# Kernel optimization log

Hardware: AMD Instinct MI355X
Metric: run time of the kernel (lower is better)

## Reference

```python
import jax, jax.numpy as jnp
import numpy as np
import math

NUM_WORDS = 8192
WORD_WIDTH = 512
PROJ_WIDTH = 64
NUM_HEADS = 8
SCALE_FACTOR = 100.0

def setup_inputs() -> dict:
    key = jax.random.key(0)
    kx, kq, kk, kv, ko = jax.random.split(key, 5)
    x = jax.random.normal(kx, (NUM_WORDS, WORD_WIDTH), dtype=jnp.float32)
    w_q = jax.random.normal(kq, (WORD_WIDTH, PROJ_WIDTH), dtype=jnp.float32) / SCALE_FACTOR
    w_k = jax.random.normal(kk, (WORD_WIDTH, PROJ_WIDTH), dtype=jnp.float32) / SCALE_FACTOR
    w_v = jax.random.normal(kv, (WORD_WIDTH, PROJ_WIDTH), dtype=jnp.float32) / SCALE_FACTOR
    w_o = jax.random.normal(ko, (WORD_WIDTH, WORD_WIDTH), dtype=jnp.float32)
    return {"x": x, "w_q": w_q, "w_k": w_k, "w_v": w_v, "w_o": w_o}

def reference(x, w_q, w_k, w_v, w_o):
    # Single self-attention head (all 8 heads in the source share the same weights).
    q = x @ w_q            # [N, P]
    k = x @ w_k            # [N, P]
    v = x @ w_v            # [N, P]
    scores = jax.nn.softmax((q @ k.T) / jnp.sqrt(jnp.float32(q.shape[1])), axis=1)  # [N, N]
    head = scores @ v      # [N, P]
    # concat of NUM_HEADS identical head outputs along dim=1
    concat = jnp.tile(head, (1, NUM_HEADS))  # [N, NUM_HEADS*P]
    return concat @ w_o    # [N, WORD_WIDTH]
```

## Files before the change

kernel.cpp:

```cpp
#include <hip/hip_runtime.h>
#include <stdint.h>

#define N_WORDS 8192
#define LOG2E_8 0.18033688011112043f

typedef __attribute__((ext_vector_type(8))) short short8;
typedef __attribute__((ext_vector_type(4))) float f32x4;
typedef __attribute__((ext_vector_type(4))) _Float16 half4;

__device__ __forceinline__ unsigned short f32_to_bf16(float f) {
    union { float f; unsigned u; } v; v.f = f;
    unsigned u = v.u;
    return (unsigned short)((u + 0x7FFFu + ((u >> 16) & 1u)) >> 16);
}

__device__ __forceinline__ unsigned short f32_to_f16(float f) {
    union { _Float16 h; unsigned short u; } cv;
    cv.h = (_Float16)f;
    return cv.u;
}

__device__ __forceinline__ void async16(const void* g, void* l) {
    __builtin_amdgcn_global_load_lds(
        (const __attribute__((address_space(1))) unsigned int*)g,
        (__attribute__((address_space(3))) unsigned int*)l, 16, 0, 0);
}

__global__ __launch_bounds__(256) void qkv_gemm(
    const float* __restrict__ x,
    const float* __restrict__ wq, const float* __restrict__ wk,
    const float* __restrict__ wv,
    unsigned short* __restrict__ qB, unsigned short* __restrict__ kB,
    unsigned short* __restrict__ vH)
{
    __shared__ __align__(16) unsigned short ldsX[64 * 72];
    __shared__ __align__(16) unsigned short ldsW[64 * 72];

    int t = threadIdx.x;
    int mt = blockIdx.x;
    int mat = blockIdx.y;
    const float* w = (mat == 0) ? wq : (mat == 1) ? wk : wv;

    int wvid = t >> 6, lane = t & 63;
    int lq = lane & 15, quad = lane >> 4;

    f32x4 acc[4];
#pragma unroll
    for (int nt = 0; nt < 4; ++nt) acc[nt] = (f32x4){0.f, 0.f, 0.f, 0.f};

    for (int kb = 0; kb < 8; ++kb) {
        int k0 = kb * 64;
        __syncthreads();
#pragma unroll
        for (int j = 0; j < 4; ++j) {
            int i = t + j * 256;
            int row = i >> 4, c4 = (i & 15) * 4;
            float4 xv = *(const float4*)(x + (size_t)(mt * 64 + row) * 512 + k0 + c4);
            unsigned p0 = f32_to_bf16(xv.x) | ((unsigned)f32_to_bf16(xv.y) << 16);
            unsigned p1 = f32_to_bf16(xv.z) | ((unsigned)f32_to_bf16(xv.w) << 16);
            *(uint2*)(&ldsX[row * 72 + c4]) = make_uint2(p0, p1);
        }
        {
            int n = t & 63, kbs = (t >> 6) * 16;
#pragma unroll
            for (int kk = 0; kk < 16; kk += 2) {
                float a = w[(size_t)(k0 + kbs + kk) * 64 + n];
                float b = w[(size_t)(k0 + kbs + kk + 1) * 64 + n];
                unsigned p = f32_to_bf16(a) | ((unsigned)f32_to_bf16(b) << 16);
                *(unsigned*)(&ldsW[n * 72 + kbs + kk]) = p;
            }
        }
        __syncthreads();

        int m = wvid * 16 + lq;
        short8 a0 = *(const short8*)(&ldsX[m * 72 + quad * 8]);
        short8 a1 = *(const short8*)(&ldsX[m * 72 + 32 + quad * 8]);
#pragma unroll
        for (int nt = 0; nt < 4; ++nt) {
            short8 b0 = *(const short8*)(&ldsW[(nt * 16 + lq) * 72 + quad * 8]);
            short8 b1 = *(const short8*)(&ldsW[(nt * 16 + lq) * 72 + 32 + quad * 8]);
            acc[nt] = __builtin_amdgcn_mfma_f32_16x16x32_bf16(a0, b0, acc[nt], 0, 0, 0);
            acc[nt] = __builtin_amdgcn_mfma_f32_16x16x32_bf16(a1, b1, acc[nt], 0, 0, 0);
        }
    }

    int mrow_base = mt * 64 + wvid * 16;
#pragma unroll
    for (int nt = 0; nt < 4; ++nt) {
#pragma unroll
        for (int r = 0; r < 4; ++r) {
            int row = mrow_base + quad * 4 + r;
            int n = nt * 16 + lq;
            float v = acc[nt][r];
            if (mat == 0) {
                v *= LOG2E_8;
                int col = ((((n >> 3) ^ (row & 7)) << 3)) | (n & 7);
                qB[(size_t)row * 64 + col] = f32_to_bf16(v);
            } else if (mat == 1) {
                int col = ((((n >> 3) ^ (row & 7)) << 3)) | (n & 7);
                kB[(size_t)row * 64 + col] = f32_to_bf16(v);
            } else {
                int rs = (row & ~63) | (((((row >> 3) & 7) ^ (n & 7)) << 3)) | (row & 7);
                vH[(size_t)n * N_WORDS + rs] = f32_to_f16(v);
            }
        }
    }
}

__global__ __launch_bounds__(256) void woeff_kernel(
    const float* __restrict__ wo, float* __restrict__ we)
{
    int i = blockIdx.x * 256 + threadIdx.x;
    int p = i >> 9;
    int j = i & 511;
    float s = 0.0f;
#pragma unroll
    for (int h = 0; h < 8; ++h) s += wo[(size_t)(h * 64 + p) * 512 + j];
    we[i] = s;
}

__global__ __launch_bounds__(256) void attn_kernel(
    const unsigned short* __restrict__ qB,
    const unsigned short* __restrict__ kB,
    const unsigned short* __restrict__ vH,
    float* __restrict__ pO, float* __restrict__ pl, int nk)
{
    __shared__ __align__(16) unsigned short ldsK[128 * 64];
    __shared__ __align__(16) unsigned short ldsV[64 * 128];

    int t = threadIdx.x;
    int wvid = t >> 6, lane = t & 63;
    int lq = lane & 15, quad = lane >> 4;
    int mbase = blockIdx.x * 128 + wvid * 32;
    int n0 = blockIdx.y * nk;

    short8 qf[2][2];
#pragma unroll
    for (int qs = 0; qs < 2; ++qs) {
        int row = mbase + qs * 16 + lq;
        const unsigned short* qr = qB + (size_t)row * 64;
        int s7 = row & 7;
        qf[qs][0] = *(const short8*)(qr + ((quad ^ s7) << 3));
        qf[qs][1] = *(const short8*)(qr + (((4 + quad) ^ s7) << 3));
    }

    f32x4 oacc[2][4];
#pragma unroll
    for (int qs = 0; qs < 2; ++qs)
#pragma unroll
        for (int vt = 0; vt < 4; ++vt) oacc[qs][vt] = (f32x4){0.f, 0.f, 0.f, 0.f};
    float lsum0 = 0.f, lsum1 = 0.f;

    int tiles = nk >> 7;
    for (int tt = 0; tt < tiles; ++tt) {
        int nb = n0 + tt * 128;
        __syncthreads();
        {
            const char* gK = (const char*)kB + (size_t)nb * 128;
#pragma unroll
            for (int i = 0; i < 4; ++i) {
                int L0 = (wvid * 4 + i) * 64;
                async16(gK + (size_t)(L0 + lane) * 16, (char*)ldsK + (size_t)L0 * 16);
            }
#pragma unroll
            for (int i = 0; i < 4; ++i) {
                int L0 = (wvid * 4 + i) * 64;
                int L = L0 + lane;
                int vcol = L >> 4, ct = L & 15;
                const char* src = (const char*)vH + (size_t)vcol * 16384 +
                                  (size_t)nb * 2 + ((ct >> 3) << 7) + ((ct & 7) << 4);
                async16(src, (char*)ldsV + (size_t)L0 * 16);
            }
        }
        __syncthreads();

#pragma unroll 2
        for (int nt = 0; nt < 8; ++nt) {
            int s7 = lq & 7;
            const unsigned short* kr = ldsK + (nt * 16 + lq) * 64;
            short8 a0 = *(const short8*)(kr + ((quad ^ s7) << 3));
            short8 a1 = *(const short8*)(kr + (((4 + quad) ^ s7) << 3));
            f32x4 st0 = (f32x4){0.f, 0.f, 0.f, 0.f};
            f32x4 st1 = (f32x4){0.f, 0.f, 0.f, 0.f};
            st0 = __builtin_amdgcn_mfma_f32_16x16x32_bf16(a0, qf[0][0], st0, 0, 0, 0);
            st0 = __builtin_amdgcn_mfma_f32_16x16x32_bf16(a1, qf[0][1], st0, 0, 0, 0);
            st1 = __builtin_amdgcn_mfma_f32_16x16x32_bf16(a0, qf[1][0], st1, 0, 0, 0);
            st1 = __builtin_amdgcn_mfma_f32_16x16x32_bf16(a1, qf[1][1], st1, 0, 0, 0);

            half4 p0, p1;
#pragma unroll
            for (int r = 0; r < 4; ++r) {
                float e = exp2f(st0[r]);
                lsum0 += e;
                p0[r] = (_Float16)e;
            }
#pragma unroll
            for (int r = 0; r < 4; ++r) {
                float e = exp2f(st1[r]);
                lsum1 += e;
                p1[r] = (_Float16)e;
            }

            int ct = nt * 2 + (quad >> 1);
            int off = (quad & 1) * 4;
#pragma unroll
            for (int vt = 0; vt < 4; ++vt) {
                int vcol = vt * 16 + lq;
                int cs = (ct & 8) | ((ct & 7) ^ (vcol & 7));
                half4 vb = *(const half4*)(ldsV + vcol * 128 + (cs << 3) + off);
                oacc[0][vt] = __builtin_amdgcn_mfma_f32_16x16x16f16(p0, vb, oacc[0][vt], 0, 0, 0);
                oacc[1][vt] = __builtin_amdgcn_mfma_f32_16x16x16f16(p1, vb, oacc[1][vt], 0, 0, 0);
            }
        }
    }

    lsum0 += __shfl_xor(lsum0, 16); lsum0 += __shfl_xor(lsum0, 32);
    lsum1 += __shfl_xor(lsum1, 16); lsum1 += __shfl_xor(lsum1, 32);

    size_t obase = (size_t)blockIdx.y * N_WORDS;
    if (quad == 0) {
        pl[obase + mbase + lq] = lsum0;
        pl[obase + mbase + 16 + lq] = lsum1;
    }
#pragma unroll
    for (int qs = 0; qs < 2; ++qs)
#pragma unroll
        for (int vt = 0; vt < 4; ++vt)
#pragma unroll
            for (int r = 0; r < 4; ++r) {
                int row = mbase + qs * 16 + quad * 4 + r;
                pO[(obase + row) * 64 + vt * 16 + lq] = oacc[qs][vt][r];
            }
}

__global__ __launch_bounds__(256) void combine_kernel(
    const float* __restrict__ pO, const float* __restrict__ pl,
    float* __restrict__ head, int S)
{
    int i = blockIdx.x * 256 + threadIdx.x;
    int row = i >> 6, d = i & 63;
    float so = 0.f, sl = 0.f;
    for (int s = 0; s < S; ++s) {
        so += pO[((size_t)s * N_WORDS + row) * 64 + d];
        sl += pl[(size_t)s * N_WORDS + row];
    }
    head[i] = so / sl;
}

__global__ __launch_bounds__(256) void out_kernel(
    const float* __restrict__ head, const float* __restrict__ we,
    float* __restrict__ out)
{
    __shared__ __align__(16) float ldsHT[64 * 16];
    int t = threadIdx.x;
    int r0 = blockIdx.x * 16;
    {
        int r = t >> 4, c4 = (t & 15) * 4;
        float4 hv = *(const float4*)(head + (size_t)(r0 + r) * 64 + c4);
        ldsHT[(c4 + 0) * 16 + r] = hv.x;
        ldsHT[(c4 + 1) * 16 + r] = hv.y;
        ldsHT[(c4 + 2) * 16 + r] = hv.z;
        ldsHT[(c4 + 3) * 16 + r] = hv.w;
    }
    __syncthreads();

    int w = t >> 6, l = t & 63;
    int cg = w & 1, rg = w >> 1;
    int j0 = cg * 256 + l * 4;

    float4 acc[8];
#pragma unroll
    for (int rr = 0; rr < 8; ++rr) acc[rr] = (float4){0.f, 0.f, 0.f, 0.f};

    for (int k = 0; k < 64; ++k) {
        float4 wv = *(const float4*)(we + (size_t)k * 512 + j0);
        float4 h0 = *(const float4*)(ldsHT + k * 16 + rg * 8);
        float4 h1 = *(const float4*)(ldsHT + k * 16 + rg * 8 + 4);
        float hr[8] = {h0.x, h0.y, h0.z, h0.w, h1.x, h1.y, h1.z, h1.w};
#pragma unroll
        for (int rr = 0; rr < 8; ++rr) {
            acc[rr].x = fmaf(hr[rr], wv.x, acc[rr].x);
            acc[rr].y = fmaf(hr[rr], wv.y, acc[rr].y);
            acc[rr].z = fmaf(hr[rr], wv.z, acc[rr].z);
            acc[rr].w = fmaf(hr[rr], wv.w, acc[rr].w);
        }
    }

#pragma unroll
    for (int rr = 0; rr < 8; ++rr) {
        int row = r0 + rg * 8 + rr;
        *(float4*)(out + (size_t)row * 512 + j0) = acc[rr];
    }
}

extern "C" void kernel_launch(void* const* d_in, const int* in_sizes, int n_in,
                              void* d_out, int out_size, void* d_ws, size_t ws_size,
                              hipStream_t stream)
{
    const float* x  = (const float*)d_in[0];
    const float* wq = (const float*)d_in[1];
    const float* wk = (const float*)d_in[2];
    const float* wv = (const float*)d_in[3];
    const float* wo = (const float*)d_in[4];
    float* out = (float*)d_out;

    char* ws = (char*)d_ws;
    unsigned short* qB = (unsigned short*)(ws);
    unsigned short* kB = (unsigned short*)(ws + 1048576);
    unsigned short* vH = (unsigned short*)(ws + 2097152);
    float* we   = (float*)(ws + 3145728);
    float* head = (float*)(ws + 3276800);
    float* pl   = (float*)(ws + 5373952);
    float* pO   = (float*)(ws + 5636096);

    int S = (ws_size >= (size_t)(5636096) + 8u * 2097152u) ? 8 : 4;
    int nk = N_WORDS / S;

    hipLaunchKernelGGL(qkv_gemm, dim3(128, 3), dim3(256), 0, stream,
                       x, wq, wk, wv, qB, kB, vH);
    hipLaunchKernelGGL(woeff_kernel, dim3(128), dim3(256), 0, stream, wo, we);
    hipLaunchKernelGGL(attn_kernel, dim3(64, S), dim3(256), 0, stream,
                       qB, kB, vH, pO, pl, nk);
    hipLaunchKernelGGL(combine_kernel, dim3(2048), dim3(256), 0, stream,
                       pO, pl, head, S);
    hipLaunchKernelGGL(out_kernel, dim3(512), dim3(256), 0, stream,
                       head, we, out);
}
```

Measured before the change: 136.9 us.

## Pre-convert inputs, double-buffer QKV and attention loads, fuse combine into output GEMM

Adds separate kernels that convert x and the Q/K/V weights to swizzled bf16 once. The QKV GEMM now computes all three projections per 16-row block and stages tiles through double-buffered async LDS copies. The attention kernel moves to 64-key tiles with double-buffered K/V staging, so the next tile's loads overlap the current tile's compute. The combine kernel is folded into the output projection, dropping one launch and the head round trip, at the cost of two extra prep launches and more workspace.

```diff
diff --git a/kernel.cpp b/kernel.cpp
--- a/kernel.cpp
+++ b/kernel.cpp
@@ -26,85 +26,41 @@
         (__attribute__((address_space(3))) unsigned int*)l, 16, 0, 0);
 }
 
-__global__ __launch_bounds__(256) void qkv_gemm(
-    const float* __restrict__ x,
+__global__ __launch_bounds__(256) void xcvt_kernel(
+    const float* __restrict__ x, unsigned short* __restrict__ xb)
+{
+    int ci = blockIdx.x * 256 + threadIdx.x;
+    int row = ci >> 6, c = ci & 63;
+    const float* src = x + ((size_t)row * 512 + c * 8);
+    float4 v0 = *(const float4*)(src);
+    float4 v1 = *(const float4*)(src + 4);
+    unsigned u0 = f32_to_bf16(v0.x) | ((unsigned)f32_to_bf16(v0.y) << 16);
+    unsigned u1 = f32_to_bf16(v0.z) | ((unsigned)f32_to_bf16(v0.w) << 16);
+    unsigned u2 = f32_to_bf16(v1.x) | ((unsigned)f32_to_bf16(v1.y) << 16);
+    unsigned u3 = f32_to_bf16(v1.z) | ((unsigned)f32_to_bf16(v1.w) << 16);
+    int dst = (c & ~7) | ((c ^ (row & 7)) & 7);
+    *(uint4*)(xb + (size_t)row * 512 + dst * 8) = make_uint4(u0, u1, u2, u3);
+}
+
+__global__ __launch_bounds__(192) void wprep_kernel(
     const float* __restrict__ wq, const float* __restrict__ wk,
-    const float* __restrict__ wv,
-    unsigned short* __restrict__ qB, unsigned short* __restrict__ kB,
-    unsigned short* __restrict__ vH)
-{
-    __shared__ __align__(16) unsigned short ldsX[64 * 72];
-    __shared__ __align__(16) unsigned short ldsW[64 * 72];
-
-    int t = threadIdx.x;
-    int mt = blockIdx.x;
-    int mat = blockIdx.y;
-    const float* w = (mat == 0) ? wq : (mat == 1) ? wk : wv;
-
-    int wvid = t >> 6, lane = t & 63;
-    int lq = lane & 15, quad = lane >> 4;
-
-    f32x4 acc[4];
-#pragma unroll
-    for (int nt = 0; nt < 4; ++nt) acc[nt] = (f32x4){0.f, 0.f, 0.f, 0.f};
-
-    for (int kb = 0; kb < 8; ++kb) {
-        int k0 = kb * 64;
-        __syncthreads();
-#pragma unroll
-        for (int j = 0; j < 4; ++j) {
-            int i = t + j * 256;
-            int row = i >> 4, c4 = (i & 15) * 4;
-            float4 xv = *(const float4*)(x + (size_t)(mt * 64 + row) * 512 + k0 + c4);
-            unsigned p0 = f32_to_bf16(xv.x) | ((unsigned)f32_to_bf16(xv.y) << 16);
-            unsigned p1 = f32_to_bf16(xv.z) | ((unsigned)f32_to_bf16(xv.w) << 16);
-            *(uint2*)(&ldsX[row * 72 + c4]) = make_uint2(p0, p1);
-        }
-        {
-            int n = t & 63, kbs = (t >> 6) * 16;
-#pragma unroll
-            for (int kk = 0; kk < 16; kk += 2) {
-                float a = w[(size_t)(k0 + kbs + kk) * 64 + n];
-                float b = w[(size_t)(k0 + kbs + kk + 1) * 64 + n];
-                unsigned p = f32_to_bf16(a) | ((unsigned)f32_to_bf16(b) << 16);
-                *(unsigned*)(&ldsW[n * 72 + kbs + kk]) = p;
-            }
-        }
-        __syncthreads();
-
-        int m = wvid * 16 + lq;
-        short8 a0 = *(const short8*)(&ldsX[m * 72 + quad * 8]);
-        short8 a1 = *(const short8*)(&ldsX[m * 72 + 32 + quad * 8]);
-#pragma unroll
-        for (int nt = 0; nt < 4; ++nt) {
-            short8 b0 = *(const short8*)(&ldsW[(nt * 16 + lq) * 72 + quad * 8]);
-            short8 b1 = *(const short8*)(&ldsW[(nt * 16 + lq) * 72 + 32 + quad * 8]);
-            acc[nt] = __builtin_amdgcn_mfma_f32_16x16x32_bf16(a0, b0, acc[nt], 0, 0, 0);
-            acc[nt] = __builtin_amdgcn_mfma_f32_16x16x32_bf16(a1, b1, acc[nt], 0, 0, 0);
-        }
-    }
-
-    int mrow_base = mt * 64 + wvid * 16;
-#pragma unroll
-    for (int nt = 0; nt < 4; ++nt) {
-#pragma unroll
-        for (int r = 0; r < 4; ++r) {
-            int row = mrow_base + quad * 4 + r;
-            int n = nt * 16 + lq;
-            float v = acc[nt][r];
-            if (mat == 0) {
-                v *= LOG2E_8;
-                int col = ((((n >> 3) ^ (row & 7)) << 3)) | (n & 7);
-                qB[(size_t)row * 64 + col] = f32_to_bf16(v);
-            } else if (mat == 1) {
-                int col = ((((n >> 3) ^ (row & 7)) << 3)) | (n & 7);
-                kB[(size_t)row * 64 + col] = f32_to_bf16(v);
-            } else {
-                int rs = (row & ~63) | (((((row >> 3) & 7) ^ (n & 7)) << 3)) | (row & 7);
-                vH[(size_t)n * N_WORDS + rs] = f32_to_f16(v);
-            }
-        }
-    }
+    const float* __restrict__ wv, unsigned short* __restrict__ wT)
+{
+    int n = threadIdx.x;
+    int c = blockIdx.x;
+    const float* w = (n < 64) ? wq : (n < 128) ? wk : wv;
+    int col = n & 63;
+    float scale = (n < 64) ? LOG2E_8 : 1.0f;
+    unsigned short o[8];
+#pragma unroll
+    for (int j = 0; j < 8; ++j)
+        o[j] = f32_to_bf16(w[(size_t)(c * 8 + j) * 64 + col] * scale);
+    unsigned u0 = o[0] | ((unsigned)o[1] << 16);
+    unsigned u1 = o[2] | ((unsigned)o[3] << 16);
+    unsigned u2 = o[4] | ((unsigned)o[5] << 16);
+    unsigned u3 = o[6] | ((unsigned)o[7] << 16);
+    int dst = (c & ~7) | ((c ^ (n & 7)) & 7);
+    *(uint4*)(wT + (size_t)n * 512 + dst * 8) = make_uint4(u0, u1, u2, u3);
 }
 
 __global__ __launch_bounds__(256) void woeff_kernel(
@@ -117,6 +73,86 @@
 #pragma unroll
     for (int h = 0; h < 8; ++h) s += wo[(size_t)(h * 64 + p) * 512 + j];
     we[i] = s;
+}
+
+__global__ __launch_bounds__(256) void qkv_gemm(
+    const unsigned short* __restrict__ xb,
+    const unsigned short* __restrict__ wT,
+    unsigned short* __restrict__ qB, unsigned short* __restrict__ kB,
+    unsigned short* __restrict__ vH)
+{
+    __shared__ __align__(16) unsigned short ldsX[2][16 * 64];
+    __shared__ __align__(16) unsigned short ldsW[2][192 * 64];
+
+    int t = threadIdx.x;
+    int wvid = t >> 6, lane = t & 63;
+    int lq = lane & 15, quad = lane >> 4;
+    int m0 = blockIdx.x * 16;
+
+    f32x4 acc[3];
+#pragma unroll
+    for (int v = 0; v < 3; ++v) acc[v] = (f32x4){0.f, 0.f, 0.f, 0.f};
+
+    auto stage = [&](int kb, int buf) {
+        int k0 = kb * 64;
+        if (wvid < 2) {
+            int L = wvid * 64 + lane;
+            int row = m0 + (L >> 3), ct = L & 7;
+            const char* src = (const char*)xb + ((size_t)row * 512 + k0) * 2 + ct * 16;
+            async16(src, (char*)(&ldsX[buf][0]) + (size_t)(wvid * 64) * 16);
+        }
+#pragma unroll
+        for (int i = 0; i < 6; ++i) {
+            int L0 = (i * 4 + wvid) * 64;
+            int L = L0 + lane;
+            int n = L >> 3, ct = L & 7;
+            const char* src = (const char*)wT + ((size_t)n * 512 + k0) * 2 + ct * 16;
+            async16(src, (char*)(&ldsW[buf][0]) + (size_t)L0 * 16);
+        }
+    };
+
+    stage(0, 0);
+    for (int kb = 0; kb < 8; ++kb) {
+        __syncthreads();
+        if (kb < 7) stage(kb + 1, (kb + 1) & 1);
+        const unsigned short* Xb = &ldsX[kb & 1][0];
+        const unsigned short* Wb = &ldsW[kb & 1][0];
+        int s7m = lq & 7;
+        short8 a0 = *(const short8*)(Xb + lq * 64 + ((quad ^ s7m) << 3));
+        short8 a1 = *(const short8*)(Xb + lq * 64 + (((4 + quad) ^ s7m) << 3));
+#pragma unroll
+        for (int v = 0; v < 3; ++v) {
+            int n = (wvid * 3 + v) * 16 + lq;
+            const unsigned short* wr = Wb + n * 64;
+            int s7 = n & 7;
+            short8 b0 = *(const short8*)(wr + ((quad ^ s7) << 3));
+            short8 b1 = *(const short8*)(wr + (((4 + quad) ^ s7) << 3));
+            acc[v] = __builtin_amdgcn_mfma_f32_16x16x32_bf16(a0, b0, acc[v], 0, 0, 0);
+            acc[v] = __builtin_amdgcn_mfma_f32_16x16x32_bf16(a1, b1, acc[v], 0, 0, 0);
+        }
+    }
+
+#pragma unroll
+    for (int v = 0; v < 3; ++v) {
+        int n = (wvid * 3 + v) * 16 + lq;
+#pragma unroll
+        for (int r = 0; r < 4; ++r) {
+            int row = m0 + quad * 4 + r;
+            float val = acc[v][r];
+            if (n < 64) {
+                int col = ((((n >> 3) ^ (row & 7)) << 3)) | (n & 7);
+                qB[(size_t)row * 64 + col] = f32_to_bf16(val);
+            } else if (n < 128) {
+                int c = n - 64;
+                int col = ((((c >> 3) ^ (row & 7)) << 3)) | (c & 7);
+                kB[(size_t)row * 64 + col] = f32_to_bf16(val);
+            } else {
+                int c = n - 128;
+                int rs = (row & ~63) | (((((row >> 3) & 7) ^ (c & 7)) << 3)) | (row & 7);
+                vH[(size_t)c * N_WORDS + rs] = f32_to_f16(val);
+            }
+        }
+    }
 }
 
 __global__ __launch_bounds__(256) void attn_kernel(
@@ -125,8 +161,8 @@
     const unsigned short* __restrict__ vH,
     float* __restrict__ pO, float* __restrict__ pl, int nk)
 {
-    __shared__ __align__(16) unsigned short ldsK[128 * 64];
-    __shared__ __align__(16) unsigned short ldsV[64 * 128];
+    __shared__ __align__(16) unsigned short ldsK[2][64 * 64];
+    __shared__ __align__(16) unsigned short ldsV[2][64 * 64];
 
     int t = threadIdx.x;
     int wvid = t >> 6, lane = t & 63;
@@ -151,33 +187,36 @@
         for (int vt = 0; vt < 4; ++vt) oacc[qs][vt] = (f32x4){0.f, 0.f, 0.f, 0.f};
     float lsum0 = 0.f, lsum1 = 0.f;
 
-    int tiles = nk >> 7;
+    auto stage = [&](int tile, int buf) {
+        int nb = n0 + tile * 64;
+        const char* gK = (const char*)kB + (size_t)nb * 128;
+#pragma unroll
+        for (int i = 0; i < 2; ++i) {
+            int L0 = (wvid * 2 + i) * 64;
+            async16(gK + (size_t)(L0 + lane) * 16, (char*)(&ldsK[buf][0]) + (size_t)L0 * 16);
+        }
+#pragma unroll
+        for (int i = 0; i < 2; ++i) {
+            int L0 = (wvid * 2 + i) * 64;
+            int L = L0 + lane;
+            int vcol = L >> 3, ct = L & 7;
+            const char* src = (const char*)vH + (size_t)vcol * 16384 + (size_t)nb * 2 + ct * 16;
+            async16(src, (char*)(&ldsV[buf][0]) + (size_t)L0 * 16);
+        }
+    };
+
+    int tiles = nk >> 6;
+    stage(0, 0);
     for (int tt = 0; tt < tiles; ++tt) {
-        int nb = n0 + tt * 128;
         __syncthreads();
-        {
-            const char* gK = (const char*)kB + (size_t)nb * 128;
-#pragma unroll
-            for (int i = 0; i < 4; ++i) {
-                int L0 = (wvid * 4 + i) * 64;
-                async16(gK + (size_t)(L0 + lane) * 16, (char*)ldsK + (size_t)L0 * 16);
-            }
-#pragma unroll
-            for (int i = 0; i < 4; ++i) {
-                int L0 = (wvid * 4 + i) * 64;
-                int L = L0 + lane;
-                int vcol = L >> 4, ct = L & 15;
-                const char* src = (const char*)vH + (size_t)vcol * 16384 +
-                                  (size_t)nb * 2 + ((ct >> 3) << 7) + ((ct & 7) << 4);
-                async16(src, (char*)ldsV + (size_t)L0 * 16);
-            }
-        }
-        __syncthreads();
-
-#pragma unroll 2
-        for (int nt = 0; nt < 8; ++nt) {
+        if (tt + 1 < tiles) stage(tt + 1, (tt + 1) & 1);
+        const unsigned short* Kb = &ldsK[tt & 1][0];
+        const unsigned short* Vb = &ldsV[tt & 1][0];
+
+#pragma unroll
+        for (int nt = 0; nt < 4; ++nt) {
             int s7 = lq & 7;
-            const unsigned short* kr = ldsK + (nt * 16 + lq) * 64;
+            const unsigned short* kr = Kb + (nt * 16 + lq) * 64;
             short8 a0 = *(const short8*)(kr + ((quad ^ s7) << 3));
             short8 a1 = *(const short8*)(kr + (((4 + quad) ^ s7) << 3));
             f32x4 st0 = (f32x4){0.f, 0.f, 0.f, 0.f};
@@ -201,13 +240,13 @@
                 p1[r] = (_Float16)e;
             }
 
-            int ct = nt * 2 + (quad >> 1);
+            int j2 = nt * 2 + (quad >> 1);
             int off = (quad & 1) * 4;
 #pragma unroll
             for (int vt = 0; vt < 4; ++vt) {
                 int vcol = vt * 16 + lq;
-                int cs = (ct & 8) | ((ct & 7) ^ (vcol & 7));
-                half4 vb = *(const half4*)(ldsV + vcol * 128 + (cs << 3) + off);
+                int p = j2 ^ (vcol & 7);
+                half4 vb = *(const half4*)(Vb + vcol * 64 + (p << 3) + off);
                 oacc[0][vt] = __builtin_amdgcn_mfma_f32_16x16x16f16(p0, vb, oacc[0][vt], 0, 0, 0);
                 oacc[1][vt] = __builtin_amdgcn_mfma_f32_16x16x16f16(p1, vb, oacc[1][vt], 0, 0, 0);
             }
@@ -233,35 +272,32 @@
             }
 }
 
-__global__ __launch_bounds__(256) void combine_kernel(
+__global__ __launch_bounds__(256) void out_kernel(
     const float* __restrict__ pO, const float* __restrict__ pl,
-    float* __restrict__ head, int S)
-{
-    int i = blockIdx.x * 256 + threadIdx.x;
-    int row = i >> 6, d = i & 63;
-    float so = 0.f, sl = 0.f;
-    for (int s = 0; s < S; ++s) {
-        so += pO[((size_t)s * N_WORDS + row) * 64 + d];
-        sl += pl[(size_t)s * N_WORDS + row];
-    }
-    head[i] = so / sl;
-}
-
-__global__ __launch_bounds__(256) void out_kernel(
-    const float* __restrict__ head, const float* __restrict__ we,
-    float* __restrict__ out)
+    const float* __restrict__ we, float* __restrict__ out, int S)
 {
     __shared__ __align__(16) float ldsHT[64 * 16];
+    __shared__ float ldsL[16];
     int t = threadIdx.x;
     int r0 = blockIdx.x * 16;
-    {
-        int r = t >> 4, c4 = (t & 15) * 4;
-        float4 hv = *(const float4*)(head + (size_t)(r0 + r) * 64 + c4);
-        ldsHT[(c4 + 0) * 16 + r] = hv.x;
-        ldsHT[(c4 + 1) * 16 + r] = hv.y;
-        ldsHT[(c4 + 2) * 16 + r] = hv.z;
-        ldsHT[(c4 + 3) * 16 + r] = hv.w;
-    }
+    int r = t >> 4, c4 = (t & 15) * 4;
+
+    float4 a = make_float4(0.f, 0.f, 0.f, 0.f);
+    for (int s = 0; s < S; ++s) {
+        float4 pv = *(const float4*)(pO + ((size_t)s * N_WORDS + r0 + r) * 64 + c4);
+        a.x += pv.x; a.y += pv.y; a.z += pv.z; a.w += pv.w;
+    }
+    if (t < 16) {
+        float lr = 0.f;
+        for (int s = 0; s < S; ++s) lr += pl[(size_t)s * N_WORDS + r0 + t];
+        ldsL[t] = lr;
+    }
+    __syncthreads();
+    float inv = 1.0f / ldsL[r];
+    ldsHT[(c4 + 0) * 16 + r] = a.x * inv;
+    ldsHT[(c4 + 1) * 16 + r] = a.y * inv;
+    ldsHT[(c4 + 2) * 16 + r] = a.z * inv;
+    ldsHT[(c4 + 3) * 16 + r] = a.w * inv;
     __syncthreads();
 
     int w = t >> 6, l = t & 63;
@@ -270,7 +306,7 @@
 
     float4 acc[8];
 #pragma unroll
-    for (int rr = 0; rr < 8; ++rr) acc[rr] = (float4){0.f, 0.f, 0.f, 0.f};
+    for (int rr = 0; rr < 8; ++rr) acc[rr] = make_float4(0.f, 0.f, 0.f, 0.f);
 
     for (int k = 0; k < 64; ++k) {
         float4 wv = *(const float4*)(we + (size_t)k * 512 + j0);
@@ -305,24 +341,24 @@
     float* out = (float*)d_out;
 
     char* ws = (char*)d_ws;
-    unsigned short* qB = (unsigned short*)(ws);
-    unsigned short* kB = (unsigned short*)(ws + 1048576);
-    unsigned short* vH = (unsigned short*)(ws + 2097152);
-    float* we   = (float*)(ws + 3145728);
-    float* head = (float*)(ws + 3276800);
-    float* pl   = (float*)(ws + 5373952);
-    float* pO   = (float*)(ws + 5636096);
-
-    int S = (ws_size >= (size_t)(5636096) + 8u * 2097152u) ? 8 : 4;
+    unsigned short* xb = (unsigned short*)(ws);
+    unsigned short* wT = (unsigned short*)(ws + 8388608);
+    float* we = (float*)(ws + 8585216);
+    float* pl = (float*)(ws + 8716288);
+    unsigned short* qB = (unsigned short*)(ws + 8978432);
+    unsigned short* kB = (unsigned short*)(ws + 10027008);
+    unsigned short* vH = (unsigned short*)(ws + 11075584);
+    float* pO = (float*)(ws + 12124160);
+
+    int S = (ws_size >= (size_t)12124160 + 8u * 2097152u) ? 8 : 4;
     int nk = N_WORDS / S;
 
-    hipLaunchKernelGGL(qkv_gemm, dim3(128, 3), dim3(256), 0, stream,
-                       x, wq, wk, wv, qB, kB, vH);
+    hipLaunchKernelGGL(xcvt_kernel, dim3(2048), dim3(256), 0, stream, x, xb);
+    hipLaunchKernelGGL(wprep_kernel, dim3(64), dim3(192), 0, stream, wq, wk, wv, wT);
     hipLaunchKernelGGL(woeff_kernel, dim3(128), dim3(256), 0, stream, wo, we);
+    hipLaunchKernelGGL(qkv_gemm, dim3(512), dim3(256), 0, stream, xb, wT, qB, kB, vH);
     hipLaunchKernelGGL(attn_kernel, dim3(64, S), dim3(256), 0, stream,
                        qB, kB, vH, pO, pl, nk);
-    hipLaunchKernelGGL(combine_kernel, dim3(2048), dim3(256), 0, stream,
-                       pO, pl, head, S);
     hipLaunchKernelGGL(out_kernel, dim3(512), dim3(256), 0, stream,
-                       head, we, out);
-}
+                       pO, pl, we, out, S);
+}
```

After: 137.6 us. Within noise of the previous version (+0.5%).
